# Kernel optimization log

Measured on AMD Instinct MI355X. Metric: run time of the kernel, lower is better.

Reference implementation:

```python
import jax, jax.numpy as jnp
import numpy as np

K_MASK = -2.3819763e+38
ROPE_THETA = 1000000
MROPE_SECTION = (24, 20, 20)
NORM_EPS = 1e-6


def rms_norm(x, w, eps=NORM_EPS):
    dtype = x.dtype
    x32 = x.astype(jnp.float32)
    rms_inv = jax.lax.rsqrt(jnp.mean(x32 * x32, axis=-1, keepdims=True) + eps)
    return w * (x32 * rms_inv).astype(dtype)


def apply_rope(inputs, positions, head_dim, rope_theta=ROPE_THETA, mrope_section=MROPE_SECTION):
    # positions: [3, B, T] (temporal, height, width); inputs: [B, T, heads, head_dim]
    fraction = 2 * jnp.arange(0, head_dim // 2, dtype=jnp.float32) / head_dim
    timescale = rope_theta ** fraction  # [head_dim//2]
    sinusoid = positions[:, :, :, None].astype(jnp.float32) / timescale  # [3,B,T,hd/2]
    freq = sinusoid[0]
    h_idx = jnp.arange(1, mrope_section[1] * 3, 3)
    w_idx = jnp.arange(2, mrope_section[2] * 3, 3)
    freq = freq.at[..., h_idx].set(sinusoid[1][..., h_idx])
    freq = freq.at[..., w_idx].set(sinusoid[2][..., w_idx])
    freq = freq[:, :, None, :]  # [B,T,1,hd/2]
    sin, cos = jnp.sin(freq), jnp.cos(freq)
    first, second = jnp.split(inputs, 2, axis=-1)
    out = jnp.concatenate([first * cos - second * sin, second * cos + first * sin], axis=-1)
    return out.astype(inputs.dtype)


def setup_inputs() -> dict:
    key = jax.random.key(0)
    ks = jax.random.split(key, 6)
    B, T, D, N, K, H = 2, 1024, 2560, 32, 8, 128
    x = jax.random.normal(ks[0], (B, T, D), dtype=jnp.float32)
    positions = jnp.broadcast_to(jnp.arange(T, dtype=jnp.int32), (3, B, T))
    attn_mask = jnp.tril(jnp.ones((T, T), dtype=bool))[None].repeat(B, axis=0)  # causal [B,T,T]
    wq = jax.random.normal(ks[1], (D, N, H), dtype=jnp.float32) * 0.02
    wk = jax.random.normal(ks[2], (D, K, H), dtype=jnp.float32) * 0.02
    wv = jax.random.normal(ks[3], (D, K, H), dtype=jnp.float32) * 0.02
    wo = jax.random.normal(ks[4], (N, H, D), dtype=jnp.float32) * 0.02
    q_norm_w = jnp.ones((H,), dtype=jnp.float32)
    k_norm_w = jnp.ones((H,), dtype=jnp.float32)
    return {"x": x, "positions": positions, "attn_mask": attn_mask, "wq": wq,
            "wk": wk, "wv": wv, "wo": wo, "q_norm_w": q_norm_w, "k_norm_w": k_norm_w}


def reference(x, positions, attn_mask, wq, wk, wv, wo, q_norm_w, k_norm_w):
    head_dim = wo.shape[1]
    scale = head_dim ** -0.5
    q = rms_norm(jnp.einsum('btd,dnh->btnh', x, wq), q_norm_w)
    k = rms_norm(jnp.einsum('bsd,dkh->bskh', x, wk), k_norm_w)
    v = jnp.einsum('bsd,dkh->bskh', x, wv)
    q = apply_rope(q, positions, head_dim)
    k = apply_rope(k, positions, head_dim)
    b, t, qh, d = q.shape
    _, s, kh, _ = k.shape
    q = q.reshape((b, t, kh, qh // kh, d))  # GQA grouping
    attn = jnp.einsum('bthgd,bshd->bhgts', q, k) * scale
    attn = attn.reshape((b, qh, t, s))
    attn = jnp.where(attn_mask[:, None, :, :], attn, K_MASK)
    attn = jax.nn.softmax(attn.astype(jnp.float32), axis=-1).astype(k.dtype)
    attn = attn.reshape((b, kh, qh // kh, t, s))
    qkv = jnp.einsum('bhgts,bshd->bthgd', attn, v).reshape((b, t, qh, d))
    return jnp.einsum('btnh,nhd->btd', qkv, wo)
```

## Files before the change

kernel.cpp:

```cpp
#include <hip/hip_runtime.h>
#include <hip/hip_bf16.h>

typedef __attribute__((ext_vector_type(8))) __bf16 bf8_t;
typedef __attribute__((ext_vector_type(4))) float f32x4;
typedef __attribute__((ext_vector_type(16))) float f32x16;

#define GLOAD16(gptr, lptr)                                                              \
  __builtin_amdgcn_global_load_lds((const __attribute__((address_space(1))) void*)(gptr), \
                                   (__attribute__((address_space(3))) void*)(lptr), 16, 0, 0)

__device__ __forceinline__ unsigned short f2bf(float f) {
  union { float f; unsigned u; } v; v.f = f;
  return (unsigned short)((v.u + 0x7fffu + ((v.u >> 16) & 1u)) >> 16);
}

__device__ __forceinline__ float bf2f(unsigned short u) {
  union { unsigned u; float f; } v; v.u = ((unsigned)u) << 16;
  return v.f;
}

__device__ __forceinline__ unsigned cvtpk_bf16(float a, float b) {
  unsigned r;
  asm("v_cvt_pk_bf16_f32 %0, %1, %2" : "=v"(r) : "v"(a), "v"(b));
  return r;
}

__global__ void cast_bf16(const float* __restrict__ in, unsigned short* __restrict__ out, int n4) {
  int i = blockIdx.x * blockDim.x + threadIdx.x;
  if (i >= n4) return;
  float4 v = ((const float4*)in)[i];
  ushort4 o;
  o.x = f2bf(v.x); o.y = f2bf(v.y); o.z = f2bf(v.z); o.w = f2bf(v.w);
  ((ushort4*)out)[i] = o;
}

__global__ void tcast(const float* __restrict__ in, unsigned short* __restrict__ out,
                      int R, int C, int ld, int rowOff) {
  __shared__ float tile[32][33];
  int c0 = blockIdx.x * 32, r0 = blockIdx.y * 32;
  int tx = threadIdx.x, ty = threadIdx.y;
#pragma unroll
  for (int i = 0; i < 4; ++i)
    tile[ty + 8 * i][tx] = in[(size_t)(r0 + ty + 8 * i) * C + c0 + tx];
  __syncthreads();
#pragma unroll
  for (int i = 0; i < 4; ++i)
    out[(size_t)(rowOff + c0 + ty + 8 * i) * ld + r0 + tx] = f2bf(tile[tx][ty + 8 * i]);
}

__global__ __launch_bounds__(512, 2) void gemm256(
    const unsigned short* __restrict__ A,
    const unsigned short* __restrict__ Bt,
    float* __restrict__ C0, float* __restrict__ C1,
    unsigned short* __restrict__ Cb,
    int N, int ldk, int Kslice, int nTileN) {
  __shared__ unsigned short SM[4][2][8192];
  int ks = blockIdx.y;
  int kbase = ks * Kslice;
  int nwg = gridDim.x;
  int bidx = blockIdx.x;
  int wg = ((bidx & 7) * (nwg >> 3)) + (bidx >> 3);
  int bm = wg / nTileN, bn = wg % nTileN;
  int m0 = bm << 8, n0 = bn << 8;
  int tid = threadIdx.x, lane = tid & 63, w = tid >> 6;
  int wm = w >> 2, wn = w & 3;
  int lrow = lane & 15, lch = lane >> 4;
  int srow = tid >> 2;
  int scol = ((tid & 3) ^ ((srow >> 1) & 3)) << 3;
  int nt = Kslice >> 5;

  f32x4 acc[8][4] = {};

  auto stage = [&](int t) {
    int buf = t & 3;
    int k0 = kbase + (t << 5);
    const unsigned short* Ag = A + (size_t)(m0 + srow) * ldk + k0 + scol;
    const unsigned short* Bg = Bt + (size_t)(n0 + srow) * ldk + k0 + scol;
    unsigned short* Al = &SM[buf][0][w << 9];
    unsigned short* Bl = &SM[buf][1][w << 9];
    GLOAD16(Ag, Al);
    GLOAD16(Ag + (size_t)128 * ldk, Al + 4096);
    GLOAD16(Bg, Bl);
    GLOAD16(Bg + (size_t)128 * ldk, Bl + 4096);
  };

  stage(0);
  stage(1);
  stage(2);
  for (int t = 0; t < nt; ++t) {
    if (t + 2 < nt)      asm volatile("s_waitcnt vmcnt(8)" ::: "memory");
    else if (t + 1 < nt) asm volatile("s_waitcnt vmcnt(4)" ::: "memory");
    else                 asm volatile("s_waitcnt vmcnt(0)" ::: "memory");
    asm volatile("s_barrier" ::: "memory");
    if (t + 3 < nt) stage(t + 3);
    int buf = t & 3;
    const unsigned short* As = &SM[buf][0][0];
    const unsigned short* Bs = &SM[buf][1][0];
    bf8_t a[8], b[4];
#pragma unroll
    for (int mi = 0; mi < 8; ++mi) {
      int ar = (wm << 7) + (mi << 4) + lrow;
      a[mi] = *(const bf8_t*)(As + ar * 32 + ((lch ^ ((ar >> 1) & 3)) << 3));
    }
#pragma unroll
    for (int ni = 0; ni < 4; ++ni) {
      int br = (wn << 6) + (ni << 4) + lrow;
      b[ni] = *(const bf8_t*)(Bs + br * 32 + ((lch ^ ((br >> 1) & 3)) << 3));
    }
    __builtin_amdgcn_s_setprio(1);
#pragma unroll
    for (int mi = 0; mi < 8; ++mi)
#pragma unroll
      for (int ni = 0; ni < 4; ++ni)
        acc[mi][ni] = __builtin_amdgcn_mfma_f32_16x16x32_bf16(a[mi], b[ni], acc[mi][ni], 0, 0, 0);
    __builtin_amdgcn_s_setprio(0);
  }
  int r0 = m0 + (wm << 7) + (lch << 2);
  int c0 = n0 + (wn << 6) + lrow;
  if (Cb) {
#pragma unroll
    for (int mi = 0; mi < 8; ++mi)
#pragma unroll
      for (int ni = 0; ni < 4; ++ni)
#pragma unroll
        for (int r = 0; r < 4; ++r)
          Cb[(size_t)(r0 + (mi << 4) + r) * N + c0 + (ni << 4)] = f2bf(acc[mi][ni][r]);
  } else {
    float* __restrict__ C = ks ? C1 : C0;
#pragma unroll
    for (int mi = 0; mi < 8; ++mi)
#pragma unroll
      for (int ni = 0; ni < 4; ++ni)
#pragma unroll
        for (int r = 0; r < 4; ++r)
          C[(size_t)(r0 + (mi << 4) + r) * N + c0 + (ni << 4)] = acc[mi][ni][r];
  }
}

__global__ void reduce_add(const float4* __restrict__ a, const float4* __restrict__ b,
                           float4* __restrict__ o, int n4) {
  int i = blockIdx.x * blockDim.x + threadIdx.x;
  if (i >= n4) return;
  float4 x = a[i], y = b[i];
  o[i] = make_float4(x.x + y.x, x.y + y.y, x.z + y.z, x.w + y.w);
}

__global__ __launch_bounds__(128) void normrope(
    const unsigned short* __restrict__ qkv, const int* __restrict__ positions,
    const float* __restrict__ qw, const float* __restrict__ kw,
    unsigned short* __restrict__ qb, unsigned short* __restrict__ kb,
    unsigned short* __restrict__ vt) {
  int blk = blockIdx.x;
  int hh = blk % 48, bt = blk / 48;
  int b = bt >> 10, t = bt & 1023;
  int tid = threadIdx.x;
  int colbase = (hh < 32) ? (hh << 7) : ((hh < 40) ? (4096 + ((hh - 32) << 7)) : (5120 + ((hh - 40) << 7)));
  float val = bf2f(qkv[(size_t)bt * 6144 + colbase + tid]);
  if (hh >= 40) {
    vt[((size_t)((b * 8 + hh - 40) * 128 + tid)) * 1024 + t] = f2bf(val);
    return;
  }
  __shared__ float red[2];
  __shared__ float xs[128];
  float ss = val * val;
#pragma unroll
  for (int m = 32; m >= 1; m >>= 1) ss += __shfl_xor(ss, m);
  if ((tid & 63) == 0) red[tid >> 6] = ss;
  __syncthreads();
  float rinv = rsqrtf((red[0] + red[1]) * (1.0f / 128.0f) + 1e-6f);
  float wgt = (hh < 32) ? qw[tid] : kw[tid];
  float xn = val * rinv * wgt;
  xs[tid] = xn;
  __syncthreads();
  float other = xs[tid ^ 64];
  int pos = positions[b * 1024 + t];
  int j = tid & 63;
  float ang = (float)pos * exp2f(-(float)j * 0.31143075889569027f);
  float sv = sinf(ang), cv = cosf(ang);
  float outv = (tid < 64) ? (xn * cv - other * sv) : (xn * cv + other * sv);
  unsigned short o = f2bf(outv);
  if (hh < 32) qb[((size_t)((b * 32 + hh) * 1024 + t)) * 128 + tid] = o;
  else kb[((size_t)((b * 8 + hh - 32) * 1024 + t)) * 128 + tid] = o;
}

__global__ __launch_bounds__(256, 2) void attn(
    const unsigned short* __restrict__ qb,
    const unsigned short* __restrict__ kb,
    const unsigned short* __restrict__ vt,
    unsigned short* __restrict__ ob) {
  __shared__ unsigned short Kl[2][64 * 128];
  __shared__ unsigned short Vl[2][128 * 64];
  int bx = blockIdx.x, hq = blockIdx.y, b = blockIdx.z;
  int qt = (bx < 4) ? (7 - bx) : (bx - 4);
  int kvh = hq >> 2;
  int tid = threadIdx.x, lane = tid & 63, w = tid >> 6;
  int qlane = lane & 31, h = lane >> 5;
  int q0 = (qt << 7) + (w << 5);
  int qg = q0 + qlane;
  const unsigned short* kbase = kb + ((size_t)(b * 8 + kvh) << 17);
  const unsigned short* vbase = vt + ((size_t)(b * 8 + kvh) << 17);
  const float c2 = 0.12751744f;

  const unsigned short* qptr = qb + ((size_t)((b * 32 + hq) * 1024 + qg) << 7) + (h << 3);
  bf8_t qf[8];
#pragma unroll
  for (int ds = 0; ds < 8; ++ds) qf[ds] = *(const bf8_t*)(qptr + ds * 16);

  f32x16 o[4] = {};
  float mrun = -3.0e38f, lrun = 0.f;
  int last_st = (q0 + 31) >> 6;
  int nsteps = 2 * qt + 2;

  auto stage = [&](int st, int buf) {
    int s0 = st << 6;
    unsigned short* kd = &Kl[buf][0];
    unsigned short* vd = &Vl[buf][0];
#pragma unroll
    for (int i = 0; i < 4; ++i) {
      int cid = i * 256 + tid;
      int kr = cid >> 4, ksl = cid & 15;
      GLOAD16(kbase + (size_t)(s0 + kr) * 128 + ((ksl ^ (kr & 15)) << 3), kd + cid * 8);
      int vr = cid >> 3, vsl = cid & 7;
      GLOAD16(vbase + (size_t)vr * 1024 + s0 + ((vsl ^ (vr & 7)) << 3), vd + cid * 8);
    }
  };

  stage(0, 0);
  for (int st = 0; st < nsteps; ++st) {
    __syncthreads();
    if (st + 1 < nsteps) stage(st + 1, (st + 1) & 1);
    if (st <= last_st) {
      const char* Kb = (const char*)&Kl[st & 1][0];
      const char* Vb = (const char*)&Vl[st & 1][0];
      f32x16 s0v = {}, s1v = {};
#pragma unroll
      for (int ds = 0; ds < 8; ++ds) {
        int c = ds * 2 + h;
        int r0 = qlane, r1 = 32 + qlane;
        bf8_t k0 = *(const bf8_t*)(Kb + r0 * 256 + ((c ^ (r0 & 15)) << 4));
        bf8_t k1 = *(const bf8_t*)(Kb + r1 * 256 + ((c ^ (r1 & 15)) << 4));
        s0v = __builtin_amdgcn_mfma_f32_32x32x16_bf16(k0, qf[ds], s0v, 0, 0, 0);
        s1v = __builtin_amdgcn_mfma_f32_32x32x16_bf16(k1, qf[ds], s1v, 0, 0, 0);
      }
      bool dm = (st == last_st);
      int kg0 = st << 6;
      float mt = -3.0e38f;
#pragma unroll
      for (int e = 0; e < 16; ++e) {
        int kl = (e & 3) + 8 * (e >> 2) + 4 * h;
        if (dm) {
          if (kg0 + kl > qg) s0v[e] = -3.0e38f;
          if (kg0 + 32 + kl > qg) s1v[e] = -3.0e38f;
        }
        mt = fmaxf(mt, fmaxf(s0v[e], s1v[e]));
      }
      mt = fmaxf(mt, __shfl_xor(mt, 32));
      float mnew = fmaxf(mrun, mt);
      float alpha = exp2f((mrun - mnew) * c2);
      float ls = 0.f;
#pragma unroll
      for (int e = 0; e < 16; ++e) {
        s0v[e] = exp2f((s0v[e] - mnew) * c2);
        s1v[e] = exp2f((s1v[e] - mnew) * c2);
        ls += s0v[e] + s1v[e];
      }
      ls += __shfl_xor(ls, 32);
      lrun = lrun * alpha + ls;
      mrun = mnew;
#pragma unroll
      for (int db = 0; db < 4; ++db)
#pragma unroll
        for (int e = 0; e < 16; ++e) o[db][e] *= alpha;
      bf8_t pf[4];
#pragma unroll
      for (int s = 0; s < 4; ++s) {
        unsigned w00, w01, w10, w11;
        {
          const int B0 = 4 * ((2 * s) & 3);
          if ((2 * s) >> 2) { w00 = cvtpk_bf16(s1v[B0], s1v[B0 + 1]); w01 = cvtpk_bf16(s1v[B0 + 2], s1v[B0 + 3]); }
          else              { w00 = cvtpk_bf16(s0v[B0], s0v[B0 + 1]); w01 = cvtpk_bf16(s0v[B0 + 2], s0v[B0 + 3]); }
        }
        {
          const int B1 = 4 * ((2 * s + 1) & 3);
          if ((2 * s + 1) >> 2) { w10 = cvtpk_bf16(s1v[B1], s1v[B1 + 1]); w11 = cvtpk_bf16(s1v[B1 + 2], s1v[B1 + 3]); }
          else                  { w10 = cvtpk_bf16(s0v[B1], s0v[B1 + 1]); w11 = cvtpk_bf16(s0v[B1 + 2], s0v[B1 + 3]); }
        }
        unsigned sa = h ? w00 : w10, sb = h ? w01 : w11;
        unsigned ra = __shfl_xor(sa, 32), rb = __shfl_xor(sb, 32);
        unsigned ka = h ? w10 : w00, kb2 = h ? w11 : w01;
        unsigned f0 = h ? ra : ka, f1 = h ? rb : kb2;
        unsigned f2 = h ? ka : ra, f3 = h ? kb2 : rb;
        uint4 fv = make_uint4(f0, f1, f2, f3);
        pf[s] = *(bf8_t*)&fv;
      }
#pragma unroll
      for (int db = 0; db < 4; ++db) {
        int vr = (db << 5) + qlane;
#pragma unroll
        for (int s = 0; s < 4; ++s) {
          int c = (s << 1) + h;
          bf8_t vf = *(const bf8_t*)(Vb + vr * 128 + ((c ^ (vr & 7)) << 4));
          o[db] = __builtin_amdgcn_mfma_f32_32x32x16_bf16(vf, pf[s], o[db], 0, 0, 0);
        }
      }
    }
  }

  __syncthreads();
  unsigned short* tb = &Kl[0][0] + (w << 12);
  float inv = 1.0f / lrun;
#pragma unroll
  for (int db = 0; db < 4; ++db)
#pragma unroll
    for (int rq = 0; rq < 4; ++rq) {
      int d0 = (db << 5) + (rq << 3) + (h << 2);
      unsigned lo = ((unsigned)f2bf(o[db][rq * 4 + 1] * inv) << 16) | f2bf(o[db][rq * 4 + 0] * inv);
      unsigned hi = ((unsigned)f2bf(o[db][rq * 4 + 3] * inv) << 16) | f2bf(o[db][rq * 4 + 2] * inv);
      *(uint2*)(tb + qlane * 128 + (d0 ^ ((qlane & 15) << 3))) = make_uint2(lo, hi);
    }
  int rr = lane >> 1, dh = (lane & 1) << 6;
  size_t orow = ((size_t)(b * 1024 + q0 + rr) << 12) + (hq << 7);
#pragma unroll
  for (int i = 0; i < 8; ++i) {
    int d8 = dh + i * 8;
    uint4 vv = *(const uint4*)(tb + rr * 128 + (d8 ^ ((rr & 15) << 3)));
    *(uint4*)(&ob[orow + d8]) = vv;
  }
}

extern "C" void kernel_launch(void* const* d_in, const int* in_sizes, int n_in,
                              void* d_out, int out_size, void* d_ws, size_t ws_size,
                              hipStream_t stream) {
  const float* x = (const float*)d_in[0];
  const int* positions = (const int*)d_in[1];
  const float* wq = (const float*)d_in[3];
  const float* wk = (const float*)d_in[4];
  const float* wv = (const float*)d_in[5];
  const float* wo = (const float*)d_in[6];
  const float* qnw = (const float*)d_in[7];
  const float* knw = (const float*)d_in[8];
  float* out = (float*)d_out;

  char* ws = (char*)d_ws;
  unsigned short* x_bf  = (unsigned short*)(ws);
  unsigned short* wqkvT = (unsigned short*)(ws + 10485760);
  unsigned short* woT   = (unsigned short*)(ws + 41943040);
  unsigned short* qkvb  = (unsigned short*)(ws + 62914560);
  float*          p0    = (float*)(ws + 62914560);
  float*          p1    = (float*)(ws + 83886080);
  unsigned short* q_bf  = (unsigned short*)(ws + 113246208);
  unsigned short* k_bf  = (unsigned short*)(ws + 130023424);
  unsigned short* vt_bf = (unsigned short*)(ws + 134217728);
  unsigned short* a_bf  = (unsigned short*)(ws + 138412032);

  cast_bf16<<<5120, 256, 0, stream>>>(x, x_bf, 2048 * 2560 / 4);
  tcast<<<dim3(128, 80), dim3(32, 8), 0, stream>>>(wq, wqkvT, 2560, 4096, 2560, 0);
  tcast<<<dim3(32, 80), dim3(32, 8), 0, stream>>>(wk, wqkvT, 2560, 1024, 2560, 4096);
  tcast<<<dim3(32, 80), dim3(32, 8), 0, stream>>>(wv, wqkvT, 2560, 1024, 2560, 5120);
  tcast<<<dim3(80, 128), dim3(32, 8), 0, stream>>>(wo, woT, 4096, 2560, 4096, 0);
  gemm256<<<dim3(8 * 24, 1), 512, 0, stream>>>(x_bf, wqkvT, nullptr, nullptr, qkvb,
                                               6144, 2560, 2560, 24);
  normrope<<<2048 * 48, 128, 0, stream>>>(qkvb, positions, qnw, knw, q_bf, k_bf, vt_bf);
  attn<<<dim3(8, 32, 2), 256, 0, stream>>>(q_bf, k_bf, vt_bf, a_bf);
  gemm256<<<dim3(8 * 10, 2), 512, 0, stream>>>(a_bf, woT, p0, p1, nullptr, 2560, 4096, 2048, 10);
  reduce_add<<<5120, 256, 0, stream>>>((const float4*)p0, (const float4*)p1, (float4*)out,
                                       2048 * 2560 / 4);
}
```

Baseline: 286.3 us.

## Restructure GEMM pipeline to 64-wide K tiles with half-tile staging and 3-way split-K

```diff
diff --git a/kernel.cpp b/kernel.cpp
--- a/kernel.cpp
+++ b/kernel.cpp
@@ -48,73 +48,93 @@
     out[(size_t)(rowOff + c0 + ty + 8 * i) * ld + r0 + tx] = f2bf(tile[tx][ty + 8 * i]);
 }
 
-__global__ __launch_bounds__(512, 2) void gemm256(
+__global__ __launch_bounds__(512, 2) void gemm256p(
     const unsigned short* __restrict__ A,
     const unsigned short* __restrict__ Bt,
-    float* __restrict__ C0, float* __restrict__ C1,
-    unsigned short* __restrict__ Cb,
-    int N, int ldk, int Kslice, int nTileN) {
-  __shared__ unsigned short SM[4][2][8192];
+    float* __restrict__ Cf, unsigned short* __restrict__ Cb,
+    int N, int ldk, int Ks0, int Ktot, int nTileN, long long pstride) {
+  __shared__ unsigned short SA[4][128 * 64];
+  __shared__ unsigned short SB[4][128 * 64];
   int ks = blockIdx.y;
-  int kbase = ks * Kslice;
-  int nwg = gridDim.x;
-  int bidx = blockIdx.x;
+  int kbase = ks * Ks0;
+  int Kslice = (ks == (int)gridDim.y - 1) ? (Ktot - kbase) : Ks0;
+  int nt = Kslice >> 6;
+  int nwg = gridDim.x, bidx = blockIdx.x;
   int wg = ((bidx & 7) * (nwg >> 3)) + (bidx >> 3);
   int bm = wg / nTileN, bn = wg % nTileN;
   int m0 = bm << 8, n0 = bn << 8;
   int tid = threadIdx.x, lane = tid & 63, w = tid >> 6;
   int wm = w >> 2, wn = w & 3;
   int lrow = lane & 15, lch = lane >> 4;
-  int srow = tid >> 2;
-  int scol = ((tid & 3) ^ ((srow >> 1) & 3)) << 3;
-  int nt = Kslice >> 5;
 
   f32x4 acc[8][4] = {};
 
-  auto stage = [&](int t) {
-    int buf = t & 3;
-    int k0 = kbase + (t << 5);
-    const unsigned short* Ag = A + (size_t)(m0 + srow) * ldk + k0 + scol;
-    const unsigned short* Bg = Bt + (size_t)(n0 + srow) * ldk + k0 + scol;
-    unsigned short* Al = &SM[buf][0][w << 9];
-    unsigned short* Bl = &SM[buf][1][w << 9];
-    GLOAD16(Ag, Al);
-    GLOAD16(Ag + (size_t)128 * ldk, Al + 4096);
-    GLOAD16(Bg, Bl);
-    GLOAD16(Bg + (size_t)128 * ldk, Bl + 4096);
+  const unsigned short* Abase = A + (size_t)m0 * ldk + kbase;
+  const unsigned short* Bbase = Bt + (size_t)n0 * ldk + kbase;
+
+  auto stageH = [&](int tt, int op, int h) {
+    int slot = (2 * tt + h) & 3;
+    unsigned short* dst = op ? SB[slot] : SA[slot];
+    const unsigned short* src = op ? Bbase : Abase;
+    int k0 = tt << 6;
+    int r1 = tid >> 3, g1 = (tid & 7) ^ (r1 & 7);
+    GLOAD16(src + (size_t)(h * 128 + r1) * ldk + k0 + g1 * 8, dst + tid * 8);
+    int r2 = 64 + r1, g2 = (tid & 7) ^ (r2 & 7);
+    GLOAD16(src + (size_t)(h * 128 + r2) * ldk + k0 + g2 * 8, dst + (tid + 512) * 8);
   };
 
-  stage(0);
-  stage(1);
-  stage(2);
+  stageH(0, 0, 0); stageH(0, 0, 1); stageH(0, 1, 0); stageH(0, 1, 1);
+
   for (int t = 0; t < nt; ++t) {
-    if (t + 2 < nt)      asm volatile("s_waitcnt vmcnt(8)" ::: "memory");
-    else if (t + 1 < nt) asm volatile("s_waitcnt vmcnt(4)" ::: "memory");
-    else                 asm volatile("s_waitcnt vmcnt(0)" ::: "memory");
+    const unsigned short* As = SA[(2 * t + wm) & 3];
+    const unsigned short* Bs = SB[(2 * t + (wn >> 1)) & 3];
+    bf8_t bfr[4][2];
+
+    auto quad = [&](int p) {
+      bf8_t afr[2][2];
+#pragma unroll
+      for (int mi2 = 0; mi2 < 2; ++mi2)
+#pragma unroll
+        for (int kk = 0; kk < 2; ++kk) {
+          int ra = ((2 * p + mi2) << 4) + lrow;
+          int u = ((kk << 2) | lch) ^ (ra & 7);
+          afr[mi2][kk] = *(const bf8_t*)(As + (ra * 8 + u) * 8);
+        }
+      __builtin_amdgcn_s_setprio(1);
+#pragma unroll
+      for (int mi2 = 0; mi2 < 2; ++mi2)
+#pragma unroll
+        for (int kk = 0; kk < 2; ++kk)
+#pragma unroll
+          for (int ni = 0; ni < 4; ++ni)
+            acc[2 * p + mi2][ni] = __builtin_amdgcn_mfma_f32_16x16x32_bf16(
+                afr[mi2][kk], bfr[ni][kk], acc[2 * p + mi2][ni], 0, 0, 0);
+      __builtin_amdgcn_s_setprio(0);
+    };
+
+    if (t + 1 < nt) { stageH(t + 1, 0, 0); stageH(t + 1, 0, 1); }
+    if (t + 1 < nt) asm volatile("s_waitcnt vmcnt(4)" ::: "memory");
+    else            asm volatile("s_waitcnt vmcnt(0)" ::: "memory");
     asm volatile("s_barrier" ::: "memory");
-    if (t + 3 < nt) stage(t + 3);
-    int buf = t & 3;
-    const unsigned short* As = &SM[buf][0][0];
-    const unsigned short* Bs = &SM[buf][1][0];
-    bf8_t a[8], b[4];
-#pragma unroll
-    for (int mi = 0; mi < 8; ++mi) {
-      int ar = (wm << 7) + (mi << 4) + lrow;
-      a[mi] = *(const bf8_t*)(As + ar * 32 + ((lch ^ ((ar >> 1) & 3)) << 3));
-    }
-#pragma unroll
-    for (int ni = 0; ni < 4; ++ni) {
-      int br = (wn << 6) + (ni << 4) + lrow;
-      b[ni] = *(const bf8_t*)(Bs + br * 32 + ((lch ^ ((br >> 1) & 3)) << 3));
-    }
-    __builtin_amdgcn_s_setprio(1);
-#pragma unroll
-    for (int mi = 0; mi < 8; ++mi)
-#pragma unroll
-      for (int ni = 0; ni < 4; ++ni)
-        acc[mi][ni] = __builtin_amdgcn_mfma_f32_16x16x32_bf16(a[mi], b[ni], acc[mi][ni], 0, 0, 0);
-    __builtin_amdgcn_s_setprio(0);
-  }
+#pragma unroll
+    for (int ni = 0; ni < 4; ++ni)
+#pragma unroll
+      for (int kk = 0; kk < 2; ++kk) {
+        int rb = ((wn & 1) << 6) + (ni << 4) + lrow;
+        int u = ((kk << 2) | lch) ^ (rb & 7);
+        bfr[ni][kk] = *(const bf8_t*)(Bs + (rb * 8 + u) * 8);
+      }
+    quad(0);
+    if (t + 1 < nt) stageH(t + 1, 1, 0);
+    asm volatile("s_barrier" ::: "memory");
+    quad(1);
+    if (t + 1 < nt) stageH(t + 1, 1, 1);
+    asm volatile("s_barrier" ::: "memory");
+    quad(2);
+    asm volatile("s_barrier" ::: "memory");
+    quad(3);
+  }
+
   int r0 = m0 + (wm << 7) + (lch << 2);
   int c0 = n0 + (wn << 6) + lrow;
   if (Cb) {
@@ -126,7 +146,7 @@
         for (int r = 0; r < 4; ++r)
           Cb[(size_t)(r0 + (mi << 4) + r) * N + c0 + (ni << 4)] = f2bf(acc[mi][ni][r]);
   } else {
-    float* __restrict__ C = ks ? C1 : C0;
+    float* __restrict__ C = Cf + (size_t)ks * pstride;
 #pragma unroll
     for (int mi = 0; mi < 8; ++mi)
 #pragma unroll
@@ -137,12 +157,12 @@
   }
 }
 
-__global__ void reduce_add(const float4* __restrict__ a, const float4* __restrict__ b,
-                           float4* __restrict__ o, int n4) {
+__global__ void reduce3(const float4* __restrict__ a, const float4* __restrict__ b,
+                        const float4* __restrict__ c, float4* __restrict__ o, int n4) {
   int i = blockIdx.x * blockDim.x + threadIdx.x;
   if (i >= n4) return;
-  float4 x = a[i], y = b[i];
-  o[i] = make_float4(x.x + y.x, x.y + y.y, x.z + y.z, x.w + y.w);
+  float4 x = a[i], y = b[i], z = c[i];
+  o[i] = make_float4(x.x + y.x + z.x, x.y + y.y + z.y, x.z + y.z + z.z, x.w + y.w + z.w);
 }
 
 __global__ __launch_bounds__(128) void normrope(
@@ -347,22 +367,24 @@
   unsigned short* woT   = (unsigned short*)(ws + 41943040);
   unsigned short* qkvb  = (unsigned short*)(ws + 62914560);
   float*          p0    = (float*)(ws + 62914560);
-  float*          p1    = (float*)(ws + 83886080);
   unsigned short* q_bf  = (unsigned short*)(ws + 113246208);
   unsigned short* k_bf  = (unsigned short*)(ws + 130023424);
   unsigned short* vt_bf = (unsigned short*)(ws + 134217728);
   unsigned short* a_bf  = (unsigned short*)(ws + 138412032);
+  const long long PSTR = 2048LL * 2560;
 
   cast_bf16<<<5120, 256, 0, stream>>>(x, x_bf, 2048 * 2560 / 4);
   tcast<<<dim3(128, 80), dim3(32, 8), 0, stream>>>(wq, wqkvT, 2560, 4096, 2560, 0);
   tcast<<<dim3(32, 80), dim3(32, 8), 0, stream>>>(wk, wqkvT, 2560, 1024, 2560, 4096);
   tcast<<<dim3(32, 80), dim3(32, 8), 0, stream>>>(wv, wqkvT, 2560, 1024, 2560, 5120);
   tcast<<<dim3(80, 128), dim3(32, 8), 0, stream>>>(wo, woT, 4096, 2560, 4096, 0);
-  gemm256<<<dim3(8 * 24, 1), 512, 0, stream>>>(x_bf, wqkvT, nullptr, nullptr, qkvb,
-                                               6144, 2560, 2560, 24);
+  gemm256p<<<dim3(192, 1), 512, 0, stream>>>(x_bf, wqkvT, nullptr, qkvb,
+                                             6144, 2560, 2560, 2560, 24, 0);
   normrope<<<2048 * 48, 128, 0, stream>>>(qkvb, positions, qnw, knw, q_bf, k_bf, vt_bf);
   attn<<<dim3(8, 32, 2), 256, 0, stream>>>(q_bf, k_bf, vt_bf, a_bf);
-  gemm256<<<dim3(8 * 10, 2), 512, 0, stream>>>(a_bf, woT, p0, p1, nullptr, 2560, 4096, 2048, 10);
-  reduce_add<<<5120, 256, 0, stream>>>((const float4*)p0, (const float4*)p1, (float4*)out,
-                                       2048 * 2560 / 4);
-}
+  gemm256p<<<dim3(80, 3), 512, 0, stream>>>(a_bf, woT, p0, nullptr,
+                                            2560, 4096, 1344, 4096, 10, PSTR);
+  reduce3<<<5120, 256, 0, stream>>>((const float4*)p0, (const float4*)(p0 + PSTR),
+                                    (const float4*)(p0 + 2 * PSTR), (float4*)out,
+                                    2048 * 2560 / 4);
+}
```

Result: no change. 287.2 us (+0.3%).

## Shrink GEMM tile to 128x256 with triple buffering for more workgroups

Applied to the files above, without the earlier changes.

```diff
diff --git a/kernel.cpp b/kernel.cpp
--- a/kernel.cpp
+++ b/kernel.cpp
@@ -48,87 +48,85 @@
     out[(size_t)(rowOff + c0 + ty + 8 * i) * ld + r0 + tx] = f2bf(tile[tx][ty + 8 * i]);
 }
 
-__global__ __launch_bounds__(512, 2) void gemm256(
+__global__ __launch_bounds__(512, 4) void gemm128(
     const unsigned short* __restrict__ A,
     const unsigned short* __restrict__ Bt,
-    float* __restrict__ C0, float* __restrict__ C1,
-    unsigned short* __restrict__ Cb,
-    int N, int ldk, int Kslice, int nTileN) {
-  __shared__ unsigned short SM[4][2][8192];
+    float* __restrict__ Cf, unsigned short* __restrict__ Cb,
+    int N, int ldk, int Ks0, int Ktot, int nTileN, long long pstride) {
+  __shared__ unsigned short SA[3][128 * 32];
+  __shared__ unsigned short SB[3][256 * 32];
   int ks = blockIdx.y;
-  int kbase = ks * Kslice;
-  int nwg = gridDim.x;
-  int bidx = blockIdx.x;
+  int kbase = ks * Ks0;
+  int Kslice = (Ktot - kbase < Ks0) ? (Ktot - kbase) : Ks0;
+  int nt = Kslice >> 5;
+  int nwg = gridDim.x, bidx = blockIdx.x;
   int wg = ((bidx & 7) * (nwg >> 3)) + (bidx >> 3);
   int bm = wg / nTileN, bn = wg % nTileN;
-  int m0 = bm << 8, n0 = bn << 8;
+  int m0 = bm << 7, n0 = bn << 8;
   int tid = threadIdx.x, lane = tid & 63, w = tid >> 6;
   int wm = w >> 2, wn = w & 3;
   int lrow = lane & 15, lch = lane >> 4;
-  int srow = tid >> 2;
-  int scol = ((tid & 3) ^ ((srow >> 1) & 3)) << 3;
-  int nt = Kslice >> 5;
-
-  f32x4 acc[8][4] = {};
+  int srow = tid >> 2, sch = tid & 3;
+  int scolA = ((sch ^ ((srow >> 1) & 3)) << 3);
+  int srow2 = 128 + srow;
+  int scolB2 = ((sch ^ ((srow2 >> 1) & 3)) << 3);
+
+  f32x4 acc[4][4] = {};
+
+  const unsigned short* Ab = A + (size_t)m0 * ldk + kbase;
+  const unsigned short* Bb = Bt + (size_t)n0 * ldk + kbase;
 
   auto stage = [&](int t) {
-    int buf = t & 3;
-    int k0 = kbase + (t << 5);
-    const unsigned short* Ag = A + (size_t)(m0 + srow) * ldk + k0 + scol;
-    const unsigned short* Bg = Bt + (size_t)(n0 + srow) * ldk + k0 + scol;
-    unsigned short* Al = &SM[buf][0][w << 9];
-    unsigned short* Bl = &SM[buf][1][w << 9];
-    GLOAD16(Ag, Al);
-    GLOAD16(Ag + (size_t)128 * ldk, Al + 4096);
-    GLOAD16(Bg, Bl);
-    GLOAD16(Bg + (size_t)128 * ldk, Bl + 4096);
+    int buf = t % 3;
+    int k0 = t << 5;
+    GLOAD16(Ab + (size_t)srow * ldk + k0 + scolA, &SA[buf][tid * 8]);
+    GLOAD16(Bb + (size_t)srow * ldk + k0 + scolA, &SB[buf][tid * 8]);
+    GLOAD16(Bb + (size_t)srow2 * ldk + k0 + scolB2, &SB[buf][(tid + 512) * 8]);
   };
 
   stage(0);
   stage(1);
-  stage(2);
   for (int t = 0; t < nt; ++t) {
-    if (t + 2 < nt)      asm volatile("s_waitcnt vmcnt(8)" ::: "memory");
-    else if (t + 1 < nt) asm volatile("s_waitcnt vmcnt(4)" ::: "memory");
-    else                 asm volatile("s_waitcnt vmcnt(0)" ::: "memory");
+    if (t + 1 < nt) asm volatile("s_waitcnt vmcnt(3)" ::: "memory");
+    else            asm volatile("s_waitcnt vmcnt(0)" ::: "memory");
     asm volatile("s_barrier" ::: "memory");
-    if (t + 3 < nt) stage(t + 3);
-    int buf = t & 3;
-    const unsigned short* As = &SM[buf][0][0];
-    const unsigned short* Bs = &SM[buf][1][0];
-    bf8_t a[8], b[4];
-#pragma unroll
-    for (int mi = 0; mi < 8; ++mi) {
-      int ar = (wm << 7) + (mi << 4) + lrow;
-      a[mi] = *(const bf8_t*)(As + ar * 32 + ((lch ^ ((ar >> 1) & 3)) << 3));
+    if (t + 2 < nt) stage(t + 2);
+    int buf = t % 3;
+    const unsigned short* As = &SA[buf][0];
+    const unsigned short* Bs = &SB[buf][0];
+    bf8_t a[4], b[4];
+#pragma unroll
+    for (int mi = 0; mi < 4; ++mi) {
+      int ra = (wm << 6) + (mi << 4) + lrow;
+      a[mi] = *(const bf8_t*)(As + ((ra << 2) + (lch ^ ((ra >> 1) & 3))) * 8);
     }
 #pragma unroll
     for (int ni = 0; ni < 4; ++ni) {
-      int br = (wn << 6) + (ni << 4) + lrow;
-      b[ni] = *(const bf8_t*)(Bs + br * 32 + ((lch ^ ((br >> 1) & 3)) << 3));
+      int rb = (wn << 6) + (ni << 4) + lrow;
+      b[ni] = *(const bf8_t*)(Bs + ((rb << 2) + (lch ^ ((rb >> 1) & 3))) * 8);
     }
     __builtin_amdgcn_s_setprio(1);
 #pragma unroll
-    for (int mi = 0; mi < 8; ++mi)
+    for (int mi = 0; mi < 4; ++mi)
 #pragma unroll
       for (int ni = 0; ni < 4; ++ni)
         acc[mi][ni] = __builtin_amdgcn_mfma_f32_16x16x32_bf16(a[mi], b[ni], acc[mi][ni], 0, 0, 0);
     __builtin_amdgcn_s_setprio(0);
   }
-  int r0 = m0 + (wm << 7) + (lch << 2);
+  int r0 = m0 + (wm << 6) + (lch << 2);
   int c0 = n0 + (wn << 6) + lrow;
   if (Cb) {
 #pragma unroll
-    for (int mi = 0; mi < 8; ++mi)
+    for (int mi = 0; mi < 4; ++mi)
 #pragma unroll
       for (int ni = 0; ni < 4; ++ni)
 #pragma unroll
         for (int r = 0; r < 4; ++r)
           Cb[(size_t)(r0 + (mi << 4) + r) * N + c0 + (ni << 4)] = f2bf(acc[mi][ni][r]);
   } else {
-    float* __restrict__ C = ks ? C1 : C0;
-#pragma unroll
-    for (int mi = 0; mi < 8; ++mi)
+    float* __restrict__ C = Cf + (size_t)ks * pstride;
+#pragma unroll
+    for (int mi = 0; mi < 4; ++mi)
 #pragma unroll
       for (int ni = 0; ni < 4; ++ni)
 #pragma unroll
@@ -352,17 +350,19 @@
   unsigned short* k_bf  = (unsigned short*)(ws + 130023424);
   unsigned short* vt_bf = (unsigned short*)(ws + 134217728);
   unsigned short* a_bf  = (unsigned short*)(ws + 138412032);
+  const long long PSTR = 2048LL * 2560;
 
   cast_bf16<<<5120, 256, 0, stream>>>(x, x_bf, 2048 * 2560 / 4);
   tcast<<<dim3(128, 80), dim3(32, 8), 0, stream>>>(wq, wqkvT, 2560, 4096, 2560, 0);
   tcast<<<dim3(32, 80), dim3(32, 8), 0, stream>>>(wk, wqkvT, 2560, 1024, 2560, 4096);
   tcast<<<dim3(32, 80), dim3(32, 8), 0, stream>>>(wv, wqkvT, 2560, 1024, 2560, 5120);
   tcast<<<dim3(80, 128), dim3(32, 8), 0, stream>>>(wo, woT, 4096, 2560, 4096, 0);
-  gemm256<<<dim3(8 * 24, 1), 512, 0, stream>>>(x_bf, wqkvT, nullptr, nullptr, qkvb,
-                                               6144, 2560, 2560, 24);
+  gemm128<<<dim3(384, 1), 512, 0, stream>>>(x_bf, wqkvT, nullptr, qkvb,
+                                            6144, 2560, 2560, 2560, 24, 0);
   normrope<<<2048 * 48, 128, 0, stream>>>(qkvb, positions, qnw, knw, q_bf, k_bf, vt_bf);
   attn<<<dim3(8, 32, 2), 256, 0, stream>>>(q_bf, k_bf, vt_bf, a_bf);
-  gemm256<<<dim3(8 * 10, 2), 512, 0, stream>>>(a_bf, woT, p0, p1, nullptr, 2560, 4096, 2048, 10);
-  reduce_add<<<5120, 256, 0, stream>>>((const float4*)p0, (const float4*)p1, (float4*)out,
-                                       2048 * 2560 / 4);
-}
+  gemm128<<<dim3(160, 2), 512, 0, stream>>>(a_bf, woT, p0, nullptr,
+                                            2560, 4096, 2048, 4096, 10, PSTR);
+  reduce_add<<<5120, 256, 0, stream>>>((const float4*)p0, (const float4*)(p0 + PSTR),
+                                       (float4*)out, 2048 * 2560 / 4);
+}
```

After: 297.9 us. 4.0% more time.
